# Kernel optimization log

Hardware: AMD Instinct MI355X
Metric: run time of the kernel (lower is better)

Reference implementation:

```python
import jax, jax.numpy as jnp
from jax import lax
import numpy as np

N, CIN, COUT, H, W = 8, 64, 64, 256, 256
KH = KW = 3
AUX, HID = 128, 256


def setup_inputs() -> dict:
    key = jax.random.key(0)
    ks = jax.random.split(key, 12)
    k = float(np.sqrt(1.0 / (CIN * KH * KW)))
    inp = {
        "x": jax.random.normal(ks[0], (N, CIN, H, W), jnp.float32),
        "y": jax.random.normal(ks[1], (N, AUX), jnp.float32),
        "weight": jax.random.uniform(ks[2], (COUT, CIN, KH, KW), jnp.float32, -k, k),
        # modulation MLP: Linear(AUX->HID), PReLU, Linear(HID->COUT*CIN), Sigmoid
        "fc_w1": jax.random.normal(ks[3], (HID, AUX), jnp.float32) * 0.05,
        "fc_b1": jax.random.normal(ks[4], (HID,), jnp.float32) * 0.05,
        "fc_prelu": jnp.asarray(0.25, jnp.float32),
        "fc_w2": jax.random.normal(ks[5], (COUT * CIN, HID), jnp.float32) * 0.05,
        "fc_b2": jax.random.normal(ks[6], (COUT * CIN,), jnp.float32) * 0.05,
        # learned-bias MLP: Linear(AUX->HID), PReLU, Linear(HID->COUT)
        "bias_w1": jax.random.normal(ks[7], (HID, AUX), jnp.float32) * 0.05,
        "bias_b1": jax.random.normal(ks[8], (HID,), jnp.float32) * 0.05,
        "bias_prelu": jnp.asarray(0.25, jnp.float32),
        "bias_w2": jax.random.normal(ks[9], (COUT, HID), jnp.float32) * 0.05,
        "bias_b2": jax.random.normal(ks[10], (COUT,), jnp.float32) * 0.05,
    }
    return inp


def _prelu(h, a):
    return jnp.where(h >= 0, h, a * h)


def reference(x, y, weight, fc_w1, fc_b1, fc_prelu, fc_w2, fc_b2,
              bias_w1, bias_b1, bias_prelu, bias_w2, bias_b2):
    n, cin, h_, w_ = x.shape
    cout = weight.shape[0]
    # modulation factors: (N, COUT*CIN), sigmoid activation
    hm = _prelu(y @ fc_w1.T + fc_b1, fc_prelu)
    mod = jax.nn.sigmoid(hm @ fc_w2.T + fc_b2)
    # per-sample modulated kernels: (N, COUT, CIN, KH, KW)
    w_mod = mod.reshape(n, cout, cin, 1, 1) * weight
    # grouped conv with groups = batch, expressed as vmap over batch
    def conv1(xi, wi):  # xi: (CIN,H,W), wi: (COUT,CIN,KH,KW)
        return lax.conv_general_dilated(
            xi[None], wi, window_strides=(1, 1), padding=[(1, 1), (1, 1)],
            rhs_dilation=(1, 1))[0]
    out = jax.vmap(conv1)(x, w_mod)  # (N, COUT, H, W)
    # learned per-sample bias
    hb = _prelu(y @ bias_w1.T + bias_b1, bias_prelu)
    b = hb @ bias_w2.T + bias_b2  # (N, COUT)
    return out + b[:, :, None, None]
```

## Files before the change

### kernel.cpp

```cpp
#include <hip/hip_runtime.h>
#include <hip/hip_bf16.h>


typedef short bf16x8 __attribute__((ext_vector_type(8)));
typedef float f32x16 __attribute__((ext_vector_type(16)));

#define NB 8
#define CIN 64
#define COUT 64
#define HH 256
#define WW 256
#define HWP (HH * WW)
#define AUXD 128
#define HIDD 256

#define XRW8 (258 * 16)
#define XBUF (4 * XRW8)
#define WOFF0 (2 * XBUF)
#define WSLOT ((9 * 64 + 1) * 16)
#define SMEMB (WOFF0 + 2 * WSLOT)

__device__ __forceinline__ unsigned short f2bf(float f) {
    unsigned u = __builtin_bit_cast(unsigned, f);
    u += 0x7FFFu + ((u >> 16) & 1u);
    return (unsigned short)(u >> 16);
}

__device__ __forceinline__ unsigned pk2(float a, float b, float vm) {
    return (unsigned)f2bf(a * vm) | ((unsigned)f2bf(b * vm) << 16);
}

__global__ __launch_bounds__(256) void mlp_kernel(
    const float* __restrict__ y, const float* __restrict__ weight,
    const float* __restrict__ fc_w1, const float* __restrict__ fc_b1,
    const float* __restrict__ fc_prelu,
    const float* __restrict__ fc_w2, const float* __restrict__ fc_b2,
    const float* __restrict__ bias_w1, const float* __restrict__ bias_b1,
    const float* __restrict__ bias_prelu,
    const float* __restrict__ bias_w2, const float* __restrict__ bias_b2,
    unsigned short* __restrict__ w_bf, float* __restrict__ bvec)
{
    const int n = blockIdx.y;
    const int c = blockIdx.x;
    const int tid = threadIdx.x;
    __shared__ float ylds[AUXD];
    __shared__ float hl[HIDD];
    if (tid < AUXD) ylds[tid] = y[n * AUXD + tid];
    __syncthreads();

    if (c < 16) {
        float s = fc_b1[tid];
        const float* wrow = fc_w1 + tid * AUXD;
        #pragma unroll 4
        for (int a = 0; a < AUXD; ++a) s += ylds[a] * wrow[a];
        float ap = fc_prelu[0];
        hl[tid] = s >= 0.f ? s : ap * s;
        __syncthreads();

        int o = c * 256 + tid;
        float t = fc_b2[o];
        const float* w2row = fc_w2 + o * HIDD;
        #pragma unroll 4
        for (int h = 0; h < HIDD; ++h) t += hl[h] * w2row[h];
        float mod = 1.f / (1.f + expf(-t));
        int cout = o >> 6, ci = o & 63;
        int cb = ci >> 3, cl = ci & 7;
        #pragma unroll
        for (int k = 0; k < 9; ++k) {
            float wv = weight[o * 9 + k];
            w_bf[((((n * 9 + k) * 8 + cb) * 64 + cout) << 3) + cl] = f2bf(mod * wv);
        }
    } else {
        float s = bias_b1[tid];
        const float* wrow = bias_w1 + tid * AUXD;
        #pragma unroll 4
        for (int a = 0; a < AUXD; ++a) s += ylds[a] * wrow[a];
        float ap = bias_prelu[0];
        hl[tid] = s >= 0.f ? s : ap * s;
        __syncthreads();
        if (tid < COUT) {
            float t = bias_b2[tid];
            const float* w2row = bias_w2 + tid * HIDD;
            #pragma unroll 4
            for (int h = 0; h < HIDD; ++h) t += hl[h] * w2row[h];
            bvec[n * COUT + tid] = t;
        }
    }
}

#define XISSUE(stv, k, ci0) { _Pragma("unroll") \
    for (int i = 0; i < 8; ++i) stv[i] = xr[k][(size_t)((ci0) + i) * HWP]; }

#define XWRITE(stv, k, buf) { float vm = vmr[k]; uint4 v; \
    v.x = pk2(stv[0], stv[1], vm); v.y = pk2(stv[2], stv[3], vm); \
    v.z = pk2(stv[4], stv[5], vm); v.w = pk2(stv[6], stv[7], vm); \
    *(uint4*)((buf) + (rg + 2 * (k)) * XRW8 + (sw + 1) * 16) = v; }

#define WLOAD(cc) { wv0 = wsrc[((tid >> 6) << 9) + (cc) * 64 + (tid & 63)]; \
    if (tid < 64) wv1 = wsrc[4096 + (cc) * 64 + tid]; }

#define WSTORE(pp) { unsigned char* wd = smem + WOFF0 + (pp) * WSLOT; \
    *(uint4*)(wd + (tid << 4)) = wv0; \
    if (tid < 64) *(uint4*)(wd + ((512 + tid) << 4)) = wv1; }

__global__ __launch_bounds__(512, 4) void conv_kernel(
    const float* __restrict__ x, const unsigned short* __restrict__ w_bf,
    const float* __restrict__ bvec, float* __restrict__ out)
{
    __shared__ __align__(16) unsigned char smem[SMEMB];

    const int bid = blockIdx.x;
    const int n = bid & 7;
    const int h0 = (bid >> 3) * 2;

    const int tid = threadIdx.x;
    const int lane = tid & 63;
    const int wave = tid >> 6;
    const int wr = wave >> 2;
    const int wq = wave & 3;
    const int l5 = lane >> 5;
    const int l31 = lane & 31;

    const int sw = tid & 255;
    const int rg = tid >> 8;

    const float* xr[2];
    float vmr[2];
    #pragma unroll
    for (int k = 0; k < 2; ++k) {
        int r = rg + 2 * k;
        int hin = h0 - 1 + r;
        bool val = (hin >= 0) && (hin < HH);
        xr[k] = x + (size_t)n * CIN * HWP + (size_t)(val ? hin : 0) * WW + sw;
        vmr[k] = val ? 1.f : 0.f;
    }

    const uint4* wsrc = (const uint4*)w_bf + (size_t)n * (9 * 8 * 64);
    uint4 wv0, wv1;

    if (tid < 16) {
        int buf = tid >> 3, r = (tid >> 1) & 3, side = tid & 1;
        uint4 z; z.x = z.y = z.z = z.w = 0u;
        *(uint4*)(smem + buf * XBUF + r * XRW8 + (side ? 257 : 0) * 16) = z;
    }
    if (tid >= 16 && tid < 18) {
        uint4 z; z.x = z.y = z.z = z.w = 0u;
        *(uint4*)(smem + WOFF0 + (tid - 16) * WSLOT + 576 * 16) = z;
    }

    float stA[8], stB[8];
    WLOAD(0);
    XISSUE(stA, 0, 0); XWRITE(stA, 0, smem);
    XISSUE(stB, 1, 0); XWRITE(stB, 1, smem);
    WSTORE(0);
    XISSUE(stA, 0, 8);

    f32x16 acc[2][2];
    #pragma unroll
    for (int m = 0; m < 2; ++m) {
        #pragma unroll
        for (int reg = 0; reg < 16; ++reg)
            acc[m][0][reg] = bvec[n * COUT + m * 32 + (reg & 3) + 8 * (reg >> 2) + 4 * l5];
        acc[m][1] = acc[m][0];
    }

    __syncthreads();

    for (int c = 0; c < 8; ++c) {
        const int p = c & 1;
        const unsigned char* rbuf = smem + p * XBUF;
        const unsigned char* wb = smem + WOFF0 + p * WSLOT;
        unsigned char* nx = smem + (p ^ 1) * XBUF;
        const bool more = (c < 7);

        #pragma unroll
        for (int s = 0; s < 5; ++s) {
            const int ka = 2 * s;
            const int kb = (s == 4) ? 8 : 2 * s + 1;
            const int khA = ka / 3, kwA = ka % 3;
            const int khB = kb / 3, kwB = kb % 3;
            const bool solo = (s == 4);

            int au = (solo && l5) ? 576 : ((l5 ? kb : ka) * 64 + l31);
            int am = (solo && l5) ? 0 : 32;
            bf16x8 aA = *(const bf16x8*)(wb + (au << 4));
            bf16x8 aB = *(const bf16x8*)(wb + ((au + am) << 4));

            int kh = l5 ? khB : khA;
            int kw = l5 ? kwB : kwA;
            const unsigned char* bb = rbuf + (wr + kh) * XRW8;
            bf16x8 b0 = *(const bf16x8*)(bb + ((wq * 64 + l31 + kw) << 4));
            bf16x8 b1 = *(const bf16x8*)(bb + ((wq * 64 + 32 + l31 + kw) << 4));

            if (s == 0 && more) { WLOAD(c + 1); }
            if (s == 1 && more) { XWRITE(stA, 0, nx); XISSUE(stB, 1, (c + 1) * 8); }
            if (s == 3 && more) { XWRITE(stB, 1, nx);
                                  if (c < 6) { XISSUE(stA, 0, (c + 2) * 8); } }
            if (s == 4 && more) { WSTORE(p ^ 1); }

            acc[0][0] = __builtin_amdgcn_mfma_f32_32x32x16_bf16(aA, b0, acc[0][0], 0, 0, 0);
            acc[0][1] = __builtin_amdgcn_mfma_f32_32x32x16_bf16(aA, b1, acc[0][1], 0, 0, 0);
            acc[1][0] = __builtin_amdgcn_mfma_f32_32x32x16_bf16(aB, b0, acc[1][0], 0, 0, 0);
            acc[1][1] = __builtin_amdgcn_mfma_f32_32x32x16_bf16(aB, b1, acc[1][1], 0, 0, 0);
        }
        __syncthreads();
    }

    const int hout = h0 + wr;
    float* ob = out + ((size_t)n * COUT * HH + hout) * WW;
    #pragma unroll
    for (int m = 0; m < 2; ++m) {
        #pragma unroll
        for (int j = 0; j < 2; ++j) {
            int colb = wq * 64 + j * 32 + l31;
            #pragma unroll
            for (int reg = 0; reg < 16; ++reg) {
                int cout = m * 32 + (reg & 3) + 8 * (reg >> 2) + 4 * l5;
                ob[(size_t)cout * HWP + colb] = acc[m][j][reg];
            }
        }
    }
}

extern "C" void kernel_launch(void* const* d_in, const int* in_sizes, int n_in,
                              void* d_out, int out_size, void* d_ws, size_t ws_size,
                              hipStream_t stream) {
    const float* x          = (const float*)d_in[0];
    const float* y          = (const float*)d_in[1];
    const float* weight     = (const float*)d_in[2];
    const float* fc_w1      = (const float*)d_in[3];
    const float* fc_b1      = (const float*)d_in[4];
    const float* fc_prelu   = (const float*)d_in[5];
    const float* fc_w2      = (const float*)d_in[6];
    const float* fc_b2      = (const float*)d_in[7];
    const float* bias_w1    = (const float*)d_in[8];
    const float* bias_b1    = (const float*)d_in[9];
    const float* bias_prelu = (const float*)d_in[10];
    const float* bias_w2    = (const float*)d_in[11];
    const float* bias_b2    = (const float*)d_in[12];
    float* out = (float*)d_out;

    unsigned short* w_bf = (unsigned short*)d_ws;
    float* bvec = (float*)((char*)d_ws + (size_t)NB * 9 * 64 * 64 * 2);

    hipLaunchKernelGGL(mlp_kernel, dim3(17, 8), dim3(256), 0, stream,
                       y, weight, fc_w1, fc_b1, fc_prelu, fc_w2, fc_b2,
                       bias_w1, bias_b1, bias_prelu, bias_w2, bias_b2, w_bf, bvec);
    hipLaunchKernelGGL(conv_kernel, dim3(1024), dim3(512), 0, stream,
                       x, w_bf, bvec, out);
}
```

Baseline: 95.85 us.

## Process four output rows per 1024-thread block with full weight tile resident in LDS

```diff
diff --git a/kernel.cpp b/kernel.cpp
--- a/kernel.cpp
+++ b/kernel.cpp
@@ -15,10 +15,10 @@
 #define HIDD 256
 
 #define XRW8 (258 * 16)
-#define XBUF (4 * XRW8)
-#define WOFF0 (2 * XBUF)
-#define WSLOT ((9 * 64 + 1) * 16)
-#define SMEMB (WOFF0 + 2 * WSLOT)
+#define XBUF8 (6 * XRW8)
+#define WOFF (2 * XBUF8)
+#define WUNITS (9 * 8 * 64)
+#define SMEMB (WOFF + (WUNITS + 1) * 16)
 
 __device__ __forceinline__ unsigned short f2bf(float f) {
     unsigned u = __builtin_bit_cast(unsigned, f);
@@ -88,22 +88,15 @@
     }
 }
 
-#define XISSUE(stv, k, ci0) { _Pragma("unroll") \
-    for (int i = 0; i < 8; ++i) stv[i] = xr[k][(size_t)((ci0) + i) * HWP]; }
-
-#define XWRITE(stv, k, buf) { float vm = vmr[k]; uint4 v; \
-    v.x = pk2(stv[0], stv[1], vm); v.y = pk2(stv[2], stv[3], vm); \
-    v.z = pk2(stv[4], stv[5], vm); v.w = pk2(stv[6], stv[7], vm); \
-    *(uint4*)((buf) + (rg + 2 * (k)) * XRW8 + (sw + 1) * 16) = v; }
-
-#define WLOAD(cc) { wv0 = wsrc[((tid >> 6) << 9) + (cc) * 64 + (tid & 63)]; \
-    if (tid < 64) wv1 = wsrc[4096 + (cc) * 64 + tid]; }
-
-#define WSTORE(pp) { unsigned char* wd = smem + WOFF0 + (pp) * WSLOT; \
-    *(uint4*)(wd + (tid << 4)) = wv0; \
-    if (tid < 64) *(uint4*)(wd + ((512 + tid) << 4)) = wv1; }
-
-__global__ __launch_bounds__(512, 4) void conv_kernel(
+#define XISSUE(stv, xp, ci0) { _Pragma("unroll") \
+    for (int i = 0; i < 8; ++i) stv[i] = (xp)[(size_t)((ci0) + i) * HWP]; }
+
+#define XWRITE(stv, rr, vmv, buf) { uint4 v_; \
+    v_.x = pk2(stv[0], stv[1], vmv); v_.y = pk2(stv[2], stv[3], vmv); \
+    v_.z = pk2(stv[4], stv[5], vmv); v_.w = pk2(stv[6], stv[7], vmv); \
+    *(uint4*)((buf) + (rr) * XRW8 + (w + 1) * 16) = v_; }
+
+__global__ __launch_bounds__(1024, 4) void conv_kernel(
     const float* __restrict__ x, const unsigned short* __restrict__ w_bf,
     const float* __restrict__ bvec, float* __restrict__ out)
 {
@@ -111,7 +104,7 @@
 
     const int bid = blockIdx.x;
     const int n = bid & 7;
-    const int h0 = (bid >> 3) * 2;
+    const int h0 = (bid >> 3) * 4;
 
     const int tid = threadIdx.x;
     const int lane = tid & 63;
@@ -121,39 +114,42 @@
     const int l5 = lane >> 5;
     const int l31 = lane & 31;
 
-    const int sw = tid & 255;
-    const int rg = tid >> 8;
-
-    const float* xr[2];
-    float vmr[2];
-    #pragma unroll
-    for (int k = 0; k < 2; ++k) {
-        int r = rg + 2 * k;
-        int hin = h0 - 1 + r;
-        bool val = (hin >= 0) && (hin < HH);
-        xr[k] = x + (size_t)n * CIN * HWP + (size_t)(val ? hin : 0) * WW + sw;
-        vmr[k] = val ? 1.f : 0.f;
-    }
-
-    const uint4* wsrc = (const uint4*)w_bf + (size_t)n * (9 * 8 * 64);
-    uint4 wv0, wv1;
-
-    if (tid < 16) {
-        int buf = tid >> 3, r = (tid >> 1) & 3, side = tid & 1;
+    const int w = tid & 255;
+    const int r0 = tid >> 8;
+    const bool has2 = (tid < 512);
+    const int r1 = 4 + (tid >> 8);
+
+    int hin0 = h0 - 1 + r0;
+    bool v0 = (hin0 >= 0) && (hin0 < HH);
+    const float vm0 = v0 ? 1.f : 0.f;
+    const float* xp0 = x + (size_t)n * CIN * HWP + (size_t)(v0 ? hin0 : 0) * WW + w;
+    int hin1 = h0 - 1 + r1;
+    bool v1 = (hin1 >= 0) && (hin1 < HH);
+    const float vm1 = v1 ? 1.f : 0.f;
+    const float* xp1 = x + (size_t)n * CIN * HWP + (size_t)(v1 ? hin1 : 0) * WW + w;
+
+    {
+        const uint4* wsrc = (const uint4*)w_bf + (size_t)n * WUNITS;
+        #pragma unroll
+        for (int it = 0; it < 5; ++it) {
+            int u = it * 1024 + tid;
+            if (u < WUNITS) *(uint4*)(smem + WOFF + (u << 4)) = wsrc[u];
+        }
+    }
+    if (tid < 24) {
+        int buf = tid / 12, rr = (tid % 12) >> 1, side = tid & 1;
         uint4 z; z.x = z.y = z.z = z.w = 0u;
-        *(uint4*)(smem + buf * XBUF + r * XRW8 + (side ? 257 : 0) * 16) = z;
-    }
-    if (tid >= 16 && tid < 18) {
+        *(uint4*)(smem + buf * XBUF8 + rr * XRW8 + (side ? 257 : 0) * 16) = z;
+    }
+    if (tid == 24) {
         uint4 z; z.x = z.y = z.z = z.w = 0u;
-        *(uint4*)(smem + WOFF0 + (tid - 16) * WSLOT + 576 * 16) = z;
+        *(uint4*)(smem + WOFF + (WUNITS << 4)) = z;
     }
 
     float stA[8], stB[8];
-    WLOAD(0);
-    XISSUE(stA, 0, 0); XWRITE(stA, 0, smem);
-    XISSUE(stB, 1, 0); XWRITE(stB, 1, smem);
-    WSTORE(0);
-    XISSUE(stA, 0, 8);
+    XISSUE(stA, xp0, 0);
+    XWRITE(stA, r0, vm0, smem);
+    if (has2) { XISSUE(stB, xp1, 0); XWRITE(stB, r1, vm1, smem); }
 
     f32x16 acc[2][2];
     #pragma unroll
@@ -164,46 +160,52 @@
         acc[m][1] = acc[m][0];
     }
 
-    __syncthreads();
+    asm volatile("s_waitcnt lgkmcnt(0)" ::: "memory");
+    __builtin_amdgcn_s_barrier();
 
     for (int c = 0; c < 8; ++c) {
         const int p = c & 1;
-        const unsigned char* rbuf = smem + p * XBUF;
-        const unsigned char* wb = smem + WOFF0 + p * WSLOT;
-        unsigned char* nx = smem + (p ^ 1) * XBUF;
+        const unsigned char* rbuf = smem + p * XBUF8;
+        unsigned char* nx = smem + (p ^ 1) * XBUF8;
         const bool more = (c < 7);
+        const int nci = (c + 1) * 8;
 
         #pragma unroll
         for (int s = 0; s < 5; ++s) {
             const int ka = 2 * s;
             const int kb = (s == 4) ? 8 : 2 * s + 1;
+            const bool solo = (s == 4);
             const int khA = ka / 3, kwA = ka % 3;
             const int khB = kb / 3, kwB = kb % 3;
-            const bool solo = (s == 4);
-
-            int au = (solo && l5) ? 576 : ((l5 ? kb : ka) * 64 + l31);
+            const int kh = l5 ? khB : khA;
+            const int kw = l5 ? kwB : kwA;
+
+            int au = (solo && l5) ? WUNITS : ((l5 ? kb : ka) * 8 + c) * 64 + l31;
             int am = (solo && l5) ? 0 : 32;
-            bf16x8 aA = *(const bf16x8*)(wb + (au << 4));
-            bf16x8 aB = *(const bf16x8*)(wb + ((au + am) << 4));
-
-            int kh = l5 ? khB : khA;
-            int kw = l5 ? kwB : kwA;
+            bf16x8 aA = *(const bf16x8*)(smem + WOFF + (au << 4));
+            bf16x8 aB = *(const bf16x8*)(smem + WOFF + ((au + am) << 4));
+
             const unsigned char* bb = rbuf + (wr + kh) * XRW8;
             bf16x8 b0 = *(const bf16x8*)(bb + ((wq * 64 + l31 + kw) << 4));
             bf16x8 b1 = *(const bf16x8*)(bb + ((wq * 64 + 32 + l31 + kw) << 4));
 
-            if (s == 0 && more) { WLOAD(c + 1); }
-            if (s == 1 && more) { XWRITE(stA, 0, nx); XISSUE(stB, 1, (c + 1) * 8); }
-            if (s == 3 && more) { XWRITE(stB, 1, nx);
-                                  if (c < 6) { XISSUE(stA, 0, (c + 2) * 8); } }
-            if (s == 4 && more) { WSTORE(p ^ 1); }
-
+            if (more) {
+                if (s == 0)              { XISSUE(stA, xp0, nci); }
+                else if (s == 1 && has2) { XISSUE(stB, xp1, nci); }
+                else if (s == 3)         { XWRITE(stA, r0, vm0, nx); }
+                else if (s == 4 && has2) { XWRITE(stB, r1, vm1, nx); }
+            }
+
+            __builtin_amdgcn_s_setprio(1);
             acc[0][0] = __builtin_amdgcn_mfma_f32_32x32x16_bf16(aA, b0, acc[0][0], 0, 0, 0);
             acc[0][1] = __builtin_amdgcn_mfma_f32_32x32x16_bf16(aA, b1, acc[0][1], 0, 0, 0);
             acc[1][0] = __builtin_amdgcn_mfma_f32_32x32x16_bf16(aB, b0, acc[1][0], 0, 0, 0);
             acc[1][1] = __builtin_amdgcn_mfma_f32_32x32x16_bf16(aB, b1, acc[1][1], 0, 0, 0);
-        }
-        __syncthreads();
+            __builtin_amdgcn_s_setprio(0);
+        }
+
+        asm volatile("s_waitcnt lgkmcnt(0)" ::: "memory");
+        __builtin_amdgcn_s_barrier();
     }
 
     const int hout = h0 + wr;
@@ -246,6 +248,6 @@
     hipLaunchKernelGGL(mlp_kernel, dim3(17, 8), dim3(256), 0, stream,
                        y, weight, fc_w1, fc_b1, fc_prelu, fc_w2, fc_b2,
                        bias_w1, bias_b1, bias_prelu, bias_w2, bias_b2, w_bf, bvec);
-    hipLaunchKernelGGL(conv_kernel, dim3(1024), dim3(512), 0, stream,
+    hipLaunchKernelGGL(conv_kernel, dim3(512), dim3(1024), 0, stream,
                        x, w_bf, bvec, out);
 }
```

Measured after the change: 87.37 us. 1.1x faster.
